# Optimization experiments

Hardware: AMD Instinct MI355X
Metric: run time of the kernel (lower is better)

The kernel has to match this reference:

```python
import jax, jax.numpy as jnp
import numpy as np

N = 9            # digits
NC = N * N       # 81 cells
H = 128          # hidden1
B = 2048         # batch of puzzles


def _constraint_mask():
    idx = np.arange(NC)
    r, c = idx // N, idx % N
    cm = np.zeros((3, NC, NC), np.float32)
    cm[0] = (r[:, None] == r[None, :])
    cm[1] = (c[:, None] == c[None, :])
    cm[2] = ((r[:, None] // 3 == r[None, :] // 3) & (c[:, None] // 3 == c[None, :] // 3))
    return cm


def setup_inputs() -> dict:
    key = jax.random.key(0)
    k1, k2, k3, k4 = jax.random.split(key, 4)
    digits = jax.random.randint(k1, (B, NC), 0, N)
    given = (jax.random.uniform(k2, (B, NC)) < 0.45).astype(jnp.float32)
    x = jax.nn.one_hot(digits, N, dtype=jnp.float32) * given[:, :, None]
    W1 = jax.random.normal(k3, (H, 3 * N), jnp.float32) * 0.05  # torch Linear weight [out,in]
    W2 = jax.random.normal(k4, (N, H), jnp.float32) * 0.05
    return {"x": x, "W1": W1, "W2": W2,
            "constraint_mask": jnp.asarray(_constraint_mask())}


def reference(x, W1, W2, constraint_mask):
    bts = x.shape[0]
    bidx = jnp.arange(bts)

    def step(carry, _):
        xc, x_pred = carry
        # constraints[b,r,q,e] = sum_k cm[r,q,k] * x[b,k,e]   (same math as
        # (x.unsqueeze(1).unsqueeze(1) * c).sum(dim=3), without the 5D temp)
        cons = jnp.einsum('rqk,bke->brqe', constraint_mask, xc)
        f = cons.reshape(bts, NC, 3 * N)          # matches torch row-major reshape
        empty = (xc.sum(-1) == 0)                 # [b,81] empty-cell mask
        h = jax.nn.relu(f @ W1.T)                 # [b,81,H]
        y = h @ W2.T                              # [b,81,9]
        s_full = jax.nn.softmax(y, axis=-1)       # softmax over digit dim
        x_pred = jnp.where(empty[:, :, None], s_full, x_pred)
        s = jnp.where(empty[:, :, None], s_full, 0.0)
        score = s.max(-1)                         # [b,81]
        pos = s.argmax(-1)                        # [b,81] best digit per cell
        mmax = score.argmax(-1)                   # [b] most confident cell
        has_empty = empty.any(-1)                 # [b] boards with work left
        digit = pos[bidx, mmax]                   # [b]
        upd = (jax.nn.one_hot(mmax, NC, dtype=xc.dtype)[:, :, None]
               * jax.nn.one_hot(digit, N, dtype=xc.dtype)[:, None, :])
        upd = upd * has_empty[:, None, None].astype(xc.dtype)
        xc = jnp.where(upd > 0, jnp.asarray(1.0, xc.dtype), xc)  # index_put_ of ones
        return (xc, x_pred), None

    # original loops min_empty (<=81) times; iterations past min_empty are no-ops
    (xf, x_pred), _ = jax.lax.scan(step, (x, x), None, length=NC)
    return x_pred
```

## Files before the change

kernel.cpp:

```cpp
#include <hip/hip_runtime.h>
#include <cstdint>
#include <cmath>


__device__ __forceinline__ void wave_fence() {
  asm volatile("s_waitcnt lgkmcnt(0)" ::: "memory");
}

__device__ __forceinline__ int dist_row(int i) {
  int r = i / 27;
  int t = i - 27 * r;
  if (r == 0) return t / 3;
  if (r == 1) return 9 + (t % 3);
  return 12 + 3 * (t / 9) + (t % 3);
}

__global__ __launch_bounds__(64, 2)
void sudoku_solver(const float* __restrict__ x, const float* __restrict__ W1g,
                   const float* __restrict__ W2g, float* __restrict__ out) {
  __shared__ double pp[27][65];
  __shared__ float  cnt[3][9][12];
  __shared__ float  sful[21][12];
  __shared__ int    rargsL[24];
  __shared__ int    digc[81];

  const int lane = threadIdx.x;
  const int b = blockIdx.x;
  const float* xb = x + b * 729;
  float* ob = out + b * 729;

  float w1a[27], w1b[27];
  #pragma unroll
  for (int c = 0; c < 27; ++c) {
    w1a[c] = W1g[lane * 27 + c];
    w1b[c] = W1g[(lane + 64) * 27 + c];
  }
  double w2Ad[9], w2Bd[9];
  #pragma unroll
  for (int d = 0; d < 9; ++d) {
    w2Ad[d] = (double)W2g[d * 128 + lane];
    w2Bd[d] = (double)W2g[d * 128 + 64 + lane];
  }

  for (int idx = lane; idx < 3 * 9 * 12; idx += 64)
    ((float*)cnt)[idx] = 0.f;

  bool eA, eB = false;
  {
    float v[9]; int dg = -1;
    #pragma unroll
    for (int e = 0; e < 9; ++e) v[e] = xb[lane * 9 + e];
    #pragma unroll
    for (int e = 0; e < 9; ++e) { if (v[e] > 0.5f) dg = e; ob[lane * 9 + e] = v[e]; }
    eA = (dg < 0); digc[lane] = dg;
    if (lane < 17) {
      const int i2 = 64 + lane;
      float w[9]; int dg2 = -1;
      #pragma unroll
      for (int e = 0; e < 9; ++e) w[e] = xb[i2 * 9 + e];
      #pragma unroll
      for (int e = 0; e < 9; ++e) { if (w[e] > 0.5f) dg2 = e; ob[i2 * 9 + e] = w[e]; }
      eB = (dg2 < 0); digc[i2] = dg2;
    }
  }
  const int distA = dist_row(lane);
  const int distB = (lane < 17) ? dist_row(64 + lane) : 255;
  const int rr3 = lane >> 4;
  const int dl  = lane & 15;
  const bool sv = (rr3 < 3) && (dl < 9);
  const int slot = rr3 * 9 + dl;
  wave_fence();

  if (lane < 27) {
    const int g = lane / 9, gi = lane - 9 * g;
    float c9[9];
    #pragma unroll
    for (int e = 0; e < 9; ++e) c9[e] = 0.f;
    #pragma unroll
    for (int k = 0; k < 9; ++k) {
      int cell;
      if (g == 0)      cell = gi * 9 + k;
      else if (g == 1) cell = k * 9 + gi;
      else             cell = (gi / 3) * 27 + (gi % 3) * 3 + (k / 3) * 9 + (k % 3);
      const int dg = digc[cell];
      #pragma unroll
      for (int e = 0; e < 9; ++e) c9[e] += (dg == e) ? 1.f : 0.f;
    }
    #pragma unroll
    for (int e = 0; e < 9; ++e) cnt[g][gi][e] = c9[e];
  }
  wave_fence();

  double myscoreA = 0.0, myscoreB = 0.0;

  auto update_rows = [&](int u0, int u1, int u2) {
    double hA[3], hB[3];
    #pragma unroll
    for (int rr = 0; rr < 3; ++rr) {
      const int u = (rr == 0) ? u0 : (rr == 1) ? u1 : u2;
      int g, gia, gib, gic;
      if (u < 9)       { g = 0; gia = gib = gic = u; }
      else if (u < 12) { g = 1; gia = 3 * (u - 9); gib = gia + 1; gic = gia + 2; }
      else             { g = 2; gia = gib = gic = u - 12; }
      const float* f0 = &cnt[g][gia][0];
      const float* f1 = &cnt[g][gib][0];
      const float* f2 = &cnt[g][gic][0];
      double a0 = 0.0, a1 = 0.0;
      #pragma unroll
      for (int c = 0; c < 9; ++c) {
        const double fv = (double)f0[c];
        a0 = fma(fv, (double)w1a[c], a0); a1 = fma(fv, (double)w1b[c], a1);
      }
      #pragma unroll
      for (int c = 0; c < 9; ++c) {
        const double fv = (double)f1[c];
        a0 = fma(fv, (double)w1a[9 + c], a0); a1 = fma(fv, (double)w1b[9 + c], a1);
      }
      #pragma unroll
      for (int c = 0; c < 9; ++c) {
        const double fv = (double)f2[c];
        a0 = fma(fv, (double)w1a[18 + c], a0); a1 = fma(fv, (double)w1b[18 + c], a1);
      }
      hA[rr] = fmax(a0, 0.0);
      hB[rr] = fmax(a1, 0.0);
    }

    #pragma unroll
    for (int rr = 0; rr < 3; ++rr)
      #pragma unroll
      for (int dd = 0; dd < 9; ++dd)
        pp[rr * 9 + dd][lane] = fma(hA[rr], w2Ad[dd], hB[rr] * w2Bd[dd]);
    wave_fence();

    double y = -1.0e300;
    if (sv) {
      double acc = 0.0;
      #pragma unroll 16
      for (int g = 0; g < 64; ++g) acc += pp[slot][g];
      y = acc;
    }

    double ymax = y;
    ymax = fmax(ymax, __shfl_xor(ymax, 1));
    ymax = fmax(ymax, __shfl_xor(ymax, 2));
    ymax = fmax(ymax, __shfl_xor(ymax, 4));
    ymax = fmax(ymax, __shfl_xor(ymax, 8));
    const double ev = sv ? exp(y - ymax) : 0.0;
    double S = ev;
    S += __shfl_xor(S, 1);
    S += __shfl_xor(S, 2);
    S += __shfl_xor(S, 4);
    S += __shfl_xor(S, 8);
    const double s = ev / S;
    const double scmp = sv ? s : -1.0;
    double smax = scmp;
    smax = fmax(smax, __shfl_xor(smax, 1));
    smax = fmax(smax, __shfl_xor(smax, 2));
    smax = fmax(smax, __shfl_xor(smax, 4));
    smax = fmax(smax, __shfl_xor(smax, 8));
    const unsigned long long bm = __ballot(scmp == smax);
    const int u_sel = (rr3 == 1) ? u1 : ((rr3 == 2) ? u2 : u0);
    if (sv) sful[u_sel][dl] = (float)s;
    if (rr3 < 3 && dl == 0)
      rargsL[u_sel] = __builtin_ctz((unsigned)((bm >> (rr3 * 16)) & 0x1FFu));

    const double sc0 = __shfl(smax, 0);
    const double sc1 = __shfl(smax, 16);
    const double sc2 = __shfl(smax, 32);
    myscoreA = (distA == u0) ? sc0 : (distA == u1) ? sc1
             : (distA == u2) ? sc2 : myscoreA;
    myscoreB = (distB == u0) ? sc0 : (distB == u1) ? sc1
             : (distB == u2) ? sc2 : myscoreB;
    wave_fence();
  };

  #pragma unroll 1
  for (int p = 0; p < 7; ++p) update_rows(3 * p, 3 * p + 1, 3 * p + 2);

  #pragma unroll 1
  for (int step = 0; step < 81; ++step) {
    const double sA = eA ? myscoreA : 0.0;
    const double sB = (lane < 17 && eB) ? myscoreB : 0.0;
    double M = fmax(sA, sB);
    M = fmax(M, __shfl_xor(M, 1));
    M = fmax(M, __shfl_xor(M, 2));
    M = fmax(M, __shfl_xor(M, 4));
    M = fmax(M, __shfl_xor(M, 8));
    M = fmax(M, __shfl_xor(M, 16));
    M = fmax(M, __shfl_xor(M, 32));
    if (M <= 0.0) break;

    const unsigned long long m0 = __ballot(sA == M);
    const unsigned long long m1 = __ballot((lane < 17) && (sB == M));
    const int mmax = m0 ? __builtin_ctzll(m0) : 64 + __builtin_ctzll(m1);

    const int du = dist_row(mmax);
    const int digit = rargsL[du];
    const int r = mmax / 9, c = mmax - 9 * r;
    const int bx = (mmax / 27) * 3 + c / 3;

    if (lane < 3) {
      const int gi = (lane == 0) ? r : (lane == 1) ? c : bx;
      cnt[lane][gi][digit] += 1.f;
    } else if (lane >= 8 && lane < 17) {
      ob[mmax * 9 + (lane - 8)] = sful[du][lane - 8];
    }
    if (lane == mmax) eA = false;
    if (lane + 64 == mmax) eB = false;
    wave_fence();

    update_rows(r, 9 + c / 3, 12 + bx);
  }
}

extern "C" void kernel_launch(void* const* d_in, const int* in_sizes, int n_in,
                              void* d_out, int out_size, void* d_ws, size_t ws_size,
                              hipStream_t stream) {
  const float* x  = (const float*)d_in[0];
  const float* W1 = (const float*)d_in[1];
  const float* W2 = (const float*)d_in[2];
  float* out = (float*)d_out;
  sudoku_solver<<<dim3(2048), dim3(64), 0, stream>>>(x, W1, W2, out);
}
```

Measured before the change: 301.1 us.

## Keep hidden pre-activations in registers and update them incrementally per placed digit

New measurement: 476.1 us. 1.58x slower.

```diff
diff --git a/kernel.cpp b/kernel.cpp
--- a/kernel.cpp
+++ b/kernel.cpp
@@ -15,10 +15,19 @@
   return 12 + 3 * (t / 9) + (t % 3);
 }
 
+#define SEL9C(A, B)                                                          \
+  (b3d ? A[(B) + 8]                                                          \
+       : (b2d ? (b1d ? (b0d ? A[(B) + 7] : A[(B) + 6])                       \
+                     : (b0d ? A[(B) + 5] : A[(B) + 4]))                      \
+              : (b1d ? (b0d ? A[(B) + 3] : A[(B) + 2])                       \
+                     : (b0d ? A[(B) + 1] : A[(B) + 0]))))
+
 __global__ __launch_bounds__(64, 2)
 void sudoku_solver(const float* __restrict__ x, const float* __restrict__ W1g,
                    const float* __restrict__ W2g, float* __restrict__ out) {
   __shared__ double pp[27][65];
+  __shared__ double ylds[32];
+  __shared__ double elds[32];
   __shared__ float  cnt[3][9][12];
   __shared__ float  sful[21][12];
   __shared__ int    rargsL[24];
@@ -65,39 +74,101 @@
   }
   const int distA = dist_row(lane);
   const int distB = (lane < 17) ? dist_row(64 + lane) : 255;
-  const int rr3 = lane >> 4;
-  const int dl  = lane & 15;
-  const bool sv = (rr3 < 3) && (dl < 9);
-  const int slot = rr3 * 9 + dl;
+  const int srow = lane / 9;
+  const int sdig = lane - 9 * srow;
   wave_fence();
 
   if (lane < 27) {
-    const int g = lane / 9, gi = lane - 9 * g;
     float c9[9];
     #pragma unroll
     for (int e = 0; e < 9; ++e) c9[e] = 0.f;
     #pragma unroll
     for (int k = 0; k < 9; ++k) {
       int cell;
-      if (g == 0)      cell = gi * 9 + k;
-      else if (g == 1) cell = k * 9 + gi;
-      else             cell = (gi / 3) * 27 + (gi % 3) * 3 + (k / 3) * 9 + (k % 3);
+      if (srow == 0)      cell = sdig * 9 + k;
+      else if (srow == 1) cell = k * 9 + sdig;
+      else cell = (sdig / 3) * 27 + (sdig % 3) * 3 + (k / 3) * 9 + (k % 3);
       const int dg = digc[cell];
       #pragma unroll
       for (int e = 0; e < 9; ++e) c9[e] += (dg == e) ? 1.f : 0.f;
     }
     #pragma unroll
-    for (int e = 0; e < 9; ++e) cnt[g][gi][e] = c9[e];
+    for (int e = 0; e < 9; ++e) cnt[srow][sdig][e] = c9[e];
   }
   wave_fence();
 
+  double pre_a[21], pre_b[21];
   double myscoreA = 0.0, myscoreB = 0.0;
 
-  auto update_rows = [&](int u0, int u1, int u2) {
-    double hA[3], hB[3];
+  auto phaseD = [&](int u0, int u1, int u2,
+                    double hA0, double hA1, double hA2,
+                    double hB0, double hB1, double hB2) {
+    #pragma unroll
+    for (int dd = 0; dd < 9; ++dd) {
+      pp[dd][lane]      = fma(hA0, w2Ad[dd], hB0 * w2Bd[dd]);
+      pp[9 + dd][lane]  = fma(hA1, w2Ad[dd], hB1 * w2Bd[dd]);
+      pp[18 + dd][lane] = fma(hA2, w2Ad[dd], hB2 * w2Bd[dd]);
+    }
+    wave_fence();
+    if (lane < 27) {
+      const double2* prow = (const double2*)&pp[lane][0];
+      double a0 = 0.0, a1 = 0.0, a2 = 0.0, a3 = 0.0;
+      #pragma unroll
+      for (int g = 0; g < 32; g += 4) {
+        const double2 v0 = prow[g],     v1 = prow[g + 1];
+        const double2 v2 = prow[g + 2], v3 = prow[g + 3];
+        a0 += v0.x + v0.y; a1 += v1.x + v1.y;
+        a2 += v2.x + v2.y; a3 += v3.x + v3.y;
+      }
+      ylds[lane] = (a0 + a1) + (a2 + a3);
+    }
+    wave_fence();
+    double S = 1.0, sval = 0.0;
+    if (lane < 27) {
+      const double* yrow = &ylds[9 * srow];
+      double y9[9];
+      #pragma unroll
+      for (int k = 0; k < 9; ++k) y9[k] = yrow[k];
+      double ymax = y9[0]; int yarg = 0;
+      #pragma unroll
+      for (int k = 1; k < 9; ++k) {
+        const bool g = y9[k] > ymax;
+        ymax = g ? y9[k] : ymax;
+        yarg = g ? k : yarg;
+      }
+      if (sdig == 0) {
+        const int us = (srow == 0) ? u0 : (srow == 1) ? u1 : u2;
+        rargsL[us] = yarg;
+      }
+      elds[lane] = exp(y9[sdig] - ymax);
+    }
+    wave_fence();
+    if (lane < 27) {
+      const double* erow = &elds[9 * srow];
+      double acc = erow[0];
+      #pragma unroll
+      for (int k = 1; k < 9; ++k) acc += erow[k];
+      S = acc;
+      sval = elds[lane] / S;
+      const int us = (srow == 0) ? u0 : (srow == 1) ? u1 : u2;
+      sful[us][sdig] = (float)sval;
+    }
+    const double sc0 = __shfl(1.0 / S, 0);
+    const double sc1 = __shfl(1.0 / S, 9);
+    const double sc2 = __shfl(1.0 / S, 18);
+    myscoreA = (distA == u0) ? sc0 : (distA == u1) ? sc1
+             : (distA == u2) ? sc2 : myscoreA;
+    myscoreB = (distB == u0) ? sc0 : (distB == u1) ? sc1
+             : (distB == u2) ? sc2 : myscoreB;
+    wave_fence();
+  };
+
+  #pragma unroll
+  for (int p = 0; p < 7; ++p) {
+    double hAv[3], hBv[3];
     #pragma unroll
     for (int rr = 0; rr < 3; ++rr) {
-      const int u = (rr == 0) ? u0 : (rr == 1) ? u1 : u2;
+      const int u = 3 * p + rr;
       int g, gia, gib, gic;
       if (u < 9)       { g = 0; gia = gib = gic = u; }
       else if (u < 12) { g = 1; gia = 3 * (u - 9); gib = gia + 1; gic = gia + 2; }
@@ -121,61 +192,12 @@
         const double fv = (double)f2[c];
         a0 = fma(fv, (double)w1a[18 + c], a0); a1 = fma(fv, (double)w1b[18 + c], a1);
       }
-      hA[rr] = fmax(a0, 0.0);
-      hB[rr] = fmax(a1, 0.0);
-    }
-
-    #pragma unroll
-    for (int rr = 0; rr < 3; ++rr)
-      #pragma unroll
-      for (int dd = 0; dd < 9; ++dd)
-        pp[rr * 9 + dd][lane] = fma(hA[rr], w2Ad[dd], hB[rr] * w2Bd[dd]);
-    wave_fence();
-
-    double y = -1.0e300;
-    if (sv) {
-      double acc = 0.0;
-      #pragma unroll 16
-      for (int g = 0; g < 64; ++g) acc += pp[slot][g];
-      y = acc;
-    }
-
-    double ymax = y;
-    ymax = fmax(ymax, __shfl_xor(ymax, 1));
-    ymax = fmax(ymax, __shfl_xor(ymax, 2));
-    ymax = fmax(ymax, __shfl_xor(ymax, 4));
-    ymax = fmax(ymax, __shfl_xor(ymax, 8));
-    const double ev = sv ? exp(y - ymax) : 0.0;
-    double S = ev;
-    S += __shfl_xor(S, 1);
-    S += __shfl_xor(S, 2);
-    S += __shfl_xor(S, 4);
-    S += __shfl_xor(S, 8);
-    const double s = ev / S;
-    const double scmp = sv ? s : -1.0;
-    double smax = scmp;
-    smax = fmax(smax, __shfl_xor(smax, 1));
-    smax = fmax(smax, __shfl_xor(smax, 2));
-    smax = fmax(smax, __shfl_xor(smax, 4));
-    smax = fmax(smax, __shfl_xor(smax, 8));
-    const unsigned long long bm = __ballot(scmp == smax);
-    const int u_sel = (rr3 == 1) ? u1 : ((rr3 == 2) ? u2 : u0);
-    if (sv) sful[u_sel][dl] = (float)s;
-    if (rr3 < 3 && dl == 0)
-      rargsL[u_sel] = __builtin_ctz((unsigned)((bm >> (rr3 * 16)) & 0x1FFu));
-
-    const double sc0 = __shfl(smax, 0);
-    const double sc1 = __shfl(smax, 16);
-    const double sc2 = __shfl(smax, 32);
-    myscoreA = (distA == u0) ? sc0 : (distA == u1) ? sc1
-             : (distA == u2) ? sc2 : myscoreA;
-    myscoreB = (distB == u0) ? sc0 : (distB == u1) ? sc1
-             : (distB == u2) ? sc2 : myscoreB;
-    wave_fence();
-  };
-
-  #pragma unroll 1
-  for (int p = 0; p < 7; ++p) update_rows(3 * p, 3 * p + 1, 3 * p + 2);
+      pre_a[u] = a0; pre_b[u] = a1;
+      hAv[rr] = fmax(a0, 0.0); hBv[rr] = fmax(a1, 0.0);
+    }
+    phaseD(3 * p, 3 * p + 1, 3 * p + 2,
+           hAv[0], hAv[1], hAv[2], hBv[0], hBv[1], hBv[2]);
+  }
 
   #pragma unroll 1
   for (int step = 0; step < 81; ++step) {
@@ -198,18 +220,44 @@
     const int digit = rargsL[du];
     const int r = mmax / 9, c = mmax - 9 * r;
     const int bx = (mmax / 27) * 3 + c / 3;
-
-    if (lane < 3) {
-      const int gi = (lane == 0) ? r : (lane == 1) ? c : bx;
-      cnt[lane][gi][digit] += 1.f;
-    } else if (lane >= 8 && lane < 17) {
+    const int q3 = c - 3 * (c / 3);
+
+    if (lane >= 8 && lane < 17)
       ob[mmax * 9 + (lane - 8)] = sful[du][lane - 8];
-    }
     if (lane == mmax) eA = false;
     if (lane + 64 == mmax) eB = false;
     wave_fence();
 
-    update_rows(r, 9 + c / 3, 12 + bx);
+    const int u0 = r, u1 = 9 + c / 3, u2 = 12 + bx;
+    const bool b0d = digit & 1, b1d = digit & 2, b2d = digit & 4, b3d = digit & 8;
+    const float ca0 = SEL9C(w1a, 0), ca1 = SEL9C(w1a, 9), ca2 = SEL9C(w1a, 18);
+    const float cb0 = SEL9C(w1b, 0), cb1 = SEL9C(w1b, 9), cb2 = SEL9C(w1b, 18);
+    const double d02a = (double)ca0 + (double)ca1 + (double)ca2;
+    const double d02b = (double)cb0 + (double)cb1 + (double)cb2;
+    const double d1a = (double)((q3 == 0) ? ca0 : ((q3 == 1) ? ca1 : ca2));
+    const double d1b = (double)((q3 == 0) ? cb0 : ((q3 == 1) ? cb1 : cb2));
+
+    double hA0 = 0.0, hB0 = 0.0, hA1 = 0.0, hB1 = 0.0, hA2 = 0.0, hB2 = 0.0;
+    #pragma unroll
+    for (int u = 0; u < 9; ++u)
+      if (u == u0) {
+        pre_a[u] += d02a; pre_b[u] += d02b;
+        hA0 = fmax(pre_a[u], 0.0); hB0 = fmax(pre_b[u], 0.0);
+      }
+    #pragma unroll
+    for (int u = 9; u < 12; ++u)
+      if (u == u1) {
+        pre_a[u] += d1a; pre_b[u] += d1b;
+        hA1 = fmax(pre_a[u], 0.0); hB1 = fmax(pre_b[u], 0.0);
+      }
+    #pragma unroll
+    for (int u = 12; u < 21; ++u)
+      if (u == u2) {
+        pre_a[u] += d02a; pre_b[u] += d02b;
+        hA2 = fmax(pre_a[u], 0.0); hB2 = fmax(pre_b[u], 0.0);
+      }
+
+    phaseD(u0, u1, u2, hA0, hA1, hA2, hB0, hB1, hB2);
   }
 }
 
```
